# Kernel tuning notes

Measured on AMD Instinct MI355X. Metric: run time of the kernel, lower is better.

Reference implementation:

```python
import jax, jax.numpy as jnp
import numpy as np

B_SZ, L, H, P = 8, 8192, 1024, 64  # batch, seq, d_inner, ssm_size
CONJ_SYM = True
DT_MIN, DT_MAX, DT_FLOOR = 1e-3, 1e-1, 1e-4


def setup_inputs() -> dict:
    key = jax.random.key(0)
    ks = jax.random.split(key, 8)
    u = jax.random.normal(ks[0], (B_SZ, L, H), dtype=jnp.float32)
    h_real = jnp.zeros((B_SZ, P), dtype=jnp.float32)
    h_imag = jnp.zeros((B_SZ, P), dtype=jnp.float32)
    # HiPPO-like stable init: Re(Lambda) = -0.5, Im(Lambda) = pi*k
    A_real = -0.5 * jnp.ones((P,), dtype=jnp.float32)
    A_imag = jnp.pi * jnp.arange(P, dtype=jnp.float32)
    local_P = 2 * P if CONJ_SYM else P
    b_scale = np.sqrt(1.0 / local_P).astype(np.float32)
    c_scale = np.sqrt(1.0 / H).astype(np.float32)
    B_real = jax.random.normal(ks[1], (P, H), dtype=jnp.float32) * b_scale
    B_imag = jax.random.normal(ks[2], (P, H), dtype=jnp.float32) * b_scale
    C_real = jax.random.normal(ks[3], (H, P), dtype=jnp.float32) * c_scale
    C_imag = jax.random.normal(ks[4], (H, P), dtype=jnp.float32) * c_scale
    D = jax.random.normal(ks[5], (H,), dtype=jnp.float32)
    # torch init: dt = exp(U(log dt_min, log dt_max)).clamp(dt_floor); inv_dt = dt + log(-expm1(-dt))
    log_dt = jax.random.uniform(ks[6], (P,), dtype=jnp.float32) \
        * (np.log(DT_MAX) - np.log(DT_MIN)) + np.log(DT_MIN)
    dt0 = jnp.clip(jnp.exp(log_dt), DT_FLOOR, None)
    inv_dt = dt0 + jnp.log(-jnp.expm1(-dt0))
    return {"u": u, "h_real": h_real, "h_imag": h_imag,
            "A_real": A_real, "A_imag": A_imag,
            "B_real": B_real, "B_imag": B_imag,
            "C_real": C_real, "C_imag": C_imag,
            "D": D, "inv_dt": inv_dt}


def reference(u, h_real, h_imag, A_real, A_imag, B_real, B_imag,
              C_real, C_imag, D, inv_dt):
    A = A_real + 1j * A_imag            # (P,)
    Bm = B_real + 1j * B_imag           # (P, H)
    Cm = C_real + 1j * C_imag           # (H, P)
    dt = jax.nn.softplus(inv_dt)        # step_rescale = 1.0
    # bilinear discretization
    den = 1.0 - (dt / 2.0) * A
    dA = (1.0 + (dt / 2.0) * A) / den   # (P,)
    dB = (dt / den)[:, None] * Bm       # (P, H)
    # input projection: Bu[b,l,p] = sum_h dB[p,h] * u[b,l,h]
    Bu = jnp.einsum('blh,ph->blp', u, dB)              # complex64 (B, L, P)
    h0 = h_real + 1j * h_imag                          # (B, P)
    Bu = Bu.at[:, 0].add(dA * h0)                      # fold initial state in
    a = jnp.broadcast_to(dA, Bu.shape)
    def combine(e1, e2):
        a1, b1 = e1
        a2, b2 = e2
        return a2 * a1, a2 * b1 + b2
    _, hs = jax.lax.associative_scan(combine, (a, Bu), axis=1)  # (B, L, P)
    yc = jnp.einsum('blp,hp->blh', hs, Cm)
    scale = 2.0 if CONJ_SYM else 1.0
    y = scale * yc.real + D * u
    h_last = hs[:, -1]
    return y, h_last.real, h_last.imag
```

## Files before the change

### kernel.cpp

```cpp
#include <hip/hip_runtime.h>

typedef unsigned short ushort_t;
typedef short s8v __attribute__((ext_vector_type(8)));
typedef unsigned short ushort8 __attribute__((ext_vector_type(8)));
typedef float floatx4 __attribute__((ext_vector_type(4)));

#define MFMA16(a, b, c) __builtin_amdgcn_mfma_f32_16x16x32_bf16((a), (b), (c), 0, 0, 0)

static constexpr int B_SZ = 8;
static constexpr int L = 8192;
static constexpr int H = 1024;
static constexpr int M_TOT = B_SZ * L;
static constexpr int S_CH = 128;
static constexpr int NC = L / S_CH;

__device__ inline ushort_t f2bf(float f) {
    union { float f; unsigned u; } v; v.f = f;
    unsigned r = v.u + 0x7fffu + ((v.u >> 16) & 1u);
    return (ushort_t)(r >> 16);
}

__device__ inline unsigned cvtpk(float lo, float hi) {
    unsigned r;
    asm("v_cvt_pk_bf16_f32 %0, %1, %2" : "=v"(r) : "v"(lo), "v"(hi));
    return r;
}

typedef union { s8v v; unsigned u[4]; } u32x4;

__device__ inline void gload_lds16(const void* g, void* l) {
    __builtin_amdgcn_global_load_lds(
        (const __attribute__((address_space(1))) void*)g,
        (__attribute__((address_space(3))) void*)l, 16, 0, 0);
}

__global__ void params_kernel(const float* __restrict__ A_real,
                              const float* __restrict__ A_imag,
                              const float* __restrict__ inv_dt,
                              float* __restrict__ params,
                              float* __restrict__ dApow) {
    int p = threadIdx.x;
    float x = inv_dt[p];
    float dt = (x > 20.f) ? x : log1pf(expf(x));
    float ar = A_real[p], ai = A_imag[p];
    float dr = 1.f - 0.5f * dt * ar;
    float di = -0.5f * dt * ai;
    float inv = 1.f / fmaf(dr, dr, di * di);
    float nr = 1.f + 0.5f * dt * ar, ni = 0.5f * dt * ai;
    float dAr = (nr * dr + ni * di) * inv;
    float dAi = (ni * dr - nr * di) * inv;
    params[p]       = dAr;
    params[64 + p]  = dAi;
    params[128 + p] = dt * dr * inv;
    params[192 + p] = -dt * di * inv;
    float pr = 1.f, pi = 0.f;
    dApow[2 * p] = 1.f; dApow[2 * p + 1] = 0.f;
    for (int k = 1; k <= S_CH; k++) {
        float npr = pr * dAr - pi * dAi;
        float npi = pr * dAi + pi * dAr;
        pr = npr; pi = npi;
        dApow[k * 128 + 2 * p]     = pr;
        dApow[k * 128 + 2 * p + 1] = pi;
    }
}

__global__ void build_w(const float* __restrict__ Br, const float* __restrict__ Bi,
                        const float* __restrict__ Cr, const float* __restrict__ Ci,
                        const float* __restrict__ params,
                        ushort_t* __restrict__ W1T, ushort_t* __restrict__ CeffT) {
    int t = blockIdx.x * 256 + threadIdx.x;
    if (t < 128 * 1024) {
        int n = t >> 10, k = t & 1023;
        int p = n >> 1;
        float sr = params[128 + p], si = params[192 + p];
        float br = Br[p * 1024 + k], bi = Bi[p * 1024 + k];
        float v = (n & 1) ? (sr * bi + si * br) : (sr * br - si * bi);
        W1T[t] = f2bf(v);
    } else {
        int t2 = t - 128 * 1024;
        int ct_ti = t2 >> 9, g = t2 & 511;
        int ct = ct_ti >> 2, ti = ct_ti & 3;
        int n = g >> 2;
        int h = ct * 128 + n;
        int qq = (g & 3) ^ ((n >> 1) & 3);
        int kb = ti * 32 + qq * 8;
        ushort8 o;
        #pragma unroll
        for (int e = 0; e < 8; e++) {
            int k = kb + e;
            int p = k >> 1;
            float v = (k & 1) ? -2.f * Ci[h * 64 + p] : 2.f * Cr[h * 64 + p];
            o[e] = f2bf(v);
        }
        *(ushort8*)&CeffT[t2 * 8] = o;
    }
}

__global__ __launch_bounds__(256) void gemm1s(const float* __restrict__ u,
                                              const ushort_t* __restrict__ W1T,
                                              const float* __restrict__ params,
                                              const float* __restrict__ dApow,
                                              float* __restrict__ hloc,
                                              float* __restrict__ endbuf) {
    __shared__ __align__(16) char smem[65536];
    float* bus = (float*)smem;
    int tid = threadIdx.x;
    int wave = tid >> 6, lane = tid & 63;
    int q = lane >> 4, mn = lane & 15;
    size_t row0 = (size_t)blockIdx.x * 128;

    int srA = lane >> 3;
    int sinA = (((lane & 7) ^ srA) << 4);
    int srB = lane >> 2;
    int sinB = (lane & 3) << 4;

    floatx4 acc[2][8] = {};

    int r0 = wave * 32 + mn;
    int maskA = (r0 & 7) << 4;
    int ya0 = r0 * 128 + q * 32;
    int ya1 = (r0 + 16) * 128 + q * 32;

    #define STAGE1(buf, kk)                                                     \
        do {                                                                    \
            _Pragma("unroll")                                                   \
            for (int i_ = 0; i_ < 4; i_++) {                                    \
                int c_ = i_ * 4 + wave;                                         \
                const char* g_ = (const char*)u +                               \
                    (row0 + c_ * 8 + srA) * 4096 + (kk) * 4 + sinA;             \
                gload_lds16(g_, smem + (buf) * 16384 + c_ * 1024);              \
            }                                                                   \
            _Pragma("unroll")                                                   \
            for (int i_ = 0; i_ < 2; i_++) {                                    \
                int c_ = i_ * 4 + wave;                                         \
                const char* g_ = (const char*)W1T +                             \
                    (size_t)(c_ * 16 + srB) * 2048 + (kk) * 2 + sinB;           \
                gload_lds16(g_, smem + 32768 + (buf) * 8192 + c_ * 1024);       \
            }                                                                   \
        } while (0)

    STAGE1(0, 0);
    __syncthreads();
    int cur = 0;
    for (int t = 0; t < 32; t++) {
        if (t < 31) STAGE1(cur ^ 1, (t + 1) * 32);
        const char* abase = smem + cur * 16384;
        floatx4 v00 = *(const floatx4*)(abase + (ya0 ^ maskA));
        floatx4 v01 = *(const floatx4*)(abase + ((ya0 + 16) ^ maskA));
        floatx4 v10 = *(const floatx4*)(abase + (ya1 ^ maskA));
        floatx4 v11 = *(const floatx4*)(abase + ((ya1 + 16) ^ maskA));
        u32x4 a0, a1;
        a0.u[0] = cvtpk(v00[0], v00[1]); a0.u[1] = cvtpk(v00[2], v00[3]);
        a0.u[2] = cvtpk(v01[0], v01[1]); a0.u[3] = cvtpk(v01[2], v01[3]);
        a1.u[0] = cvtpk(v10[0], v10[1]); a1.u[1] = cvtpk(v10[2], v10[3]);
        a1.u[2] = cvtpk(v11[0], v11[1]); a1.u[3] = cvtpk(v11[2], v11[3]);
        const ushort_t* bb = (const ushort_t*)(smem + 32768 + cur * 8192);
        #pragma unroll
        for (int j = 0; j < 8; j++) {
            s8v bf = *(const s8v*)(bb + (j * 16 + mn) * 32 + q * 8);
            acc[0][j] = MFMA16(a0.v, bf, acc[0][j]);
            acc[1][j] = MFMA16(a1.v, bf, acc[1][j]);
        }
        __syncthreads();
        cur ^= 1;
    }
    #undef STAGE1

    #pragma unroll
    for (int i = 0; i < 2; i++)
        #pragma unroll
        for (int j = 0; j < 8; j++)
            #pragma unroll
            for (int reg = 0; reg < 4; reg++) {
                int row = wave * 32 + i * 16 + q * 4 + reg;
                bus[row * 128 + j * 16 + mn] = acc[i][j][reg];
            }
    __syncthreads();

    float dAr = params[lane], dAi = params[64 + lane];
    float hr = 0.f, hi = 0.f;
    int base = wave * 32 * 128 + 2 * lane;
    #pragma unroll 8
    for (int t = 0; t < 32; t++) {
        float2 v = *(float2*)&bus[base + t * 128];
        float nhr = fmaf(dAr, hr, fmaf(-dAi, hi, v.x));
        float nhi = fmaf(dAr, hi, fmaf(dAi, hr, v.y));
        hr = nhr; hi = nhi;
        *(float2*)&bus[base + t * 128] = make_float2(hr, hi);
    }
    __syncthreads();

    float a32r = dApow[32 * 128 + 2 * lane], a32i = dApow[32 * 128 + 2 * lane + 1];
    float cr = 0.f, ci = 0.f;
    for (int w2 = 0; w2 < wave; w2++) {
        float2 e = *(float2*)&bus[(w2 * 32 + 31) * 128 + 2 * lane];
        float tr = fmaf(a32r, cr, fmaf(-a32i, ci, e.x));
        float ti = fmaf(a32r, ci, fmaf(a32i, cr, e.y));
        cr = tr; ci = ti;
    }

    float* gbase = hloc + (row0 + wave * 32) * 128 + 2 * lane;
    float lr = 0.f, li = 0.f;
    float pr = dAr, pi = dAi;
    #pragma unroll 8
    for (int t = 0; t < 32; t++) {
        float2 v = *(float2*)&bus[base + t * 128];
        float orr = v.x + pr * cr - pi * ci;
        float oi  = v.y + pr * ci + pi * cr;
        *(float2*)(gbase + (size_t)t * 128) = make_float2(orr, oi);
        lr = orr; li = oi;
        float npr = pr * dAr - pi * dAi;
        float npi = pr * dAi + pi * dAr;
        pr = npr; pi = npi;
    }
    if (wave == 3) {
        float* e = endbuf + (size_t)blockIdx.x * 128 + 2 * lane;
        e[0] = lr; e[1] = li;
    }
}

__global__ void scan_carry(const float* __restrict__ endbuf,
                           const float* __restrict__ dApow,
                           const float* __restrict__ h0r,
                           const float* __restrict__ h0i,
                           float* __restrict__ carry) {
    int t = blockIdx.x * 64 + threadIdx.x;
    int b = t >> 6, p = t & 63;
    float aSr = dApow[S_CH * 128 + 2 * p], aSi = dApow[S_CH * 128 + 2 * p + 1];
    float cr = h0r[b * 64 + p], ci = h0i[b * 64 + p];
    #pragma unroll
    for (int half = 0; half < 2; half++) {
        float2 e[32];
        #pragma unroll
        for (int c = 0; c < 32; c++)
            e[c] = *(const float2*)(endbuf + ((size_t)b * NC + half * 32 + c) * 128 + 2 * p);
        #pragma unroll
        for (int c = 0; c < 32; c++) {
            int cc = half * 32 + c;
            *(float2*)(carry + ((size_t)b * NC + cc) * 128 + 2 * p) = make_float2(cr, ci);
            float nr = fmaf(aSr, cr, fmaf(-aSi, ci, e[c].x));
            float ni = fmaf(aSr, ci, fmaf(aSi, cr, e[c].y));
            cr = nr; ci = ni;
        }
    }
}

__global__ __launch_bounds__(256, 4) void gemm2t(const float* __restrict__ hloc,
                                                 const ushort_t* __restrict__ CeffT,
                                                 const float* __restrict__ u,
                                                 const float* __restrict__ D,
                                                 const float* __restrict__ dApow,
                                                 const float* __restrict__ carry,
                                                 float* __restrict__ y,
                                                 float* __restrict__ out_hlast) {
    __shared__ __align__(16) char smem[64 * 132 * 4];
    ushort_t* Blds = (ushort_t*)smem;
    float* ldsF = (float*)smem;
    int tid = threadIdx.x;
    int w = tid >> 6, lane = tid & 63;
    int q = lane >> 4, mn = lane & 15;
    int swz = q ^ ((mn >> 1) & 3);
    size_t row0 = (size_t)blockIdx.x * 64;
    int b = (int)(row0 >> 13);
    int l0 = (int)(row0 & (L - 1));
    int c = l0 >> 7;

    int seq = w * 16 + mn;
    int l = l0 + seq;
    int kp = (l & (S_CH - 1)) + 1;
    const float* hrow = hloc + (row0 + seq) * 128;
    const float* prow = dApow + (size_t)kp * 128;
    const float* crow = carry + ((size_t)b * NC + c) * 128;
    bool last = (l == L - 1);

    u32x4 Bf[4];
    #pragma unroll
    for (int kt = 0; kt < 4; kt++) {
        int kb = kt * 32 + q * 8;
        float4 h0 = *(const float4*)(hrow + kb);
        float4 h1 = *(const float4*)(hrow + kb + 4);
        float4 p0 = *(const float4*)(prow + kb);
        float4 p1 = *(const float4*)(prow + kb + 4);
        float4 c0 = *(const float4*)(crow + kb);
        float4 c1 = *(const float4*)(crow + kb + 4);
        float f0 = h0.x + p0.x * c0.x - p0.y * c0.y;
        float f1 = h0.y + p0.x * c0.y + p0.y * c0.x;
        float f2 = h0.z + p0.z * c0.z - p0.w * c0.w;
        float f3 = h0.w + p0.z * c0.w + p0.w * c0.z;
        float f4 = h1.x + p1.x * c1.x - p1.y * c1.y;
        float f5 = h1.y + p1.x * c1.y + p1.y * c1.x;
        float f6 = h1.z + p1.z * c1.z - p1.w * c1.w;
        float f7 = h1.w + p1.z * c1.w + p1.w * c1.z;
        Bf[kt].u[0] = cvtpk(f0, f1); Bf[kt].u[1] = cvtpk(f2, f3);
        Bf[kt].u[2] = cvtpk(f4, f5); Bf[kt].u[3] = cvtpk(f6, f7);
        if (last) {
            int pb = kb >> 1;
            out_hlast[b * 64 + pb]     = f0; out_hlast[512 + b * 64 + pb]     = f1;
            out_hlast[b * 64 + pb + 1] = f2; out_hlast[512 + b * 64 + pb + 1] = f3;
            out_hlast[b * 64 + pb + 2] = f4; out_hlast[512 + b * 64 + pb + 2] = f5;
            out_hlast[b * 64 + pb + 3] = f6; out_hlast[512 + b * 64 + pb + 3] = f7;
        }
    }

    int erow_b = w * 16 + (lane >> 5);
    int es4 = lane & 31;

    for (int ct = 0; ct < 8; ct++) {
        const float* ub = u + ct * 128 + es4 * 4;
        float4 uv0 = *(const float4*)(ub + (row0 + erow_b + 0) * 1024);
        float4 uv1 = *(const float4*)(ub + (row0 + erow_b + 2) * 1024);
        float4 uv2 = *(const float4*)(ub + (row0 + erow_b + 4) * 1024);
        float4 uv3 = *(const float4*)(ub + (row0 + erow_b + 6) * 1024);
        float4 dvv = *(const float4*)(D + ct * 128 + es4 * 4);

        if (ct) __syncthreads();
        {
            const ushort_t* gsrc = CeffT + (size_t)ct * 16384 + w * 512 + lane * 8;
            ushort_t* ldst = Blds + w * 512;
            #pragma unroll
            for (int it = 0; it < 8; it++)
                gload_lds16(gsrc + it * 2048, ldst + it * 2048);
        }
        __syncthreads();
        floatx4 acc[8] = {};
        #pragma unroll
        for (int kt = 0; kt < 4; kt++) {
            int bofs = kt * 4096 + swz * 8;
            #pragma unroll
            for (int j = 0; j < 8; j++) {
                s8v af = *(const s8v*)&Blds[bofs + (j * 16 + mn) * 32];
                acc[j] = MFMA16(af, Bf[kt].v, acc[j]);
            }
        }
        __syncthreads();
        #pragma unroll
        for (int j = 0; j < 8; j++)
            *(floatx4*)&ldsF[(size_t)seq * 132 + j * 16 + q * 4] = acc[j];
        __syncthreads();
        #pragma unroll
        for (int i = 0; i < 8; i++) {
            int row = erow_b + i * 2;
            float4 fv = *(const float4*)&ldsF[(size_t)row * 132 + es4 * 4];
            float4 uvv = (i == 0) ? uv0 : (i == 1) ? uv1 : (i == 2) ? uv2 :
                         (i == 3) ? uv3 :
                         *(const float4*)(ub + (row0 + row) * 1024);
            float4 o;
            o.x = fv.x + dvv.x * uvv.x;
            o.y = fv.y + dvv.y * uvv.y;
            o.z = fv.z + dvv.z * uvv.z;
            o.w = fv.w + dvv.w * uvv.w;
            *(float4*)(y + (row0 + row) * 1024 + ct * 128 + es4 * 4) = o;
        }
    }
}

extern "C" void kernel_launch(void* const* d_in, const int* in_sizes, int n_in,
                              void* d_out, int out_size, void* d_ws, size_t ws_size,
                              hipStream_t stream) {
    const float* u      = (const float*)d_in[0];
    const float* h_r    = (const float*)d_in[1];
    const float* h_i    = (const float*)d_in[2];
    const float* A_real = (const float*)d_in[3];
    const float* A_imag = (const float*)d_in[4];
    const float* B_real = (const float*)d_in[5];
    const float* B_imag = (const float*)d_in[6];
    const float* C_real = (const float*)d_in[7];
    const float* C_imag = (const float*)d_in[8];
    const float* D      = (const float*)d_in[9];
    const float* inv_dt = (const float*)d_in[10];
    float* out = (float*)d_out;

    float* wsf       = (float*)d_ws;
    float* P_params  = wsf;
    float* P_dApow   = wsf + 1024;
    float* P_carry   = wsf + 1024 + 16640;
    float* P_end     = P_carry + 65536;
    ushort_t* P_W1T  = (ushort_t*)(P_end + 65536);
    ushort_t* P_Ceff = P_W1T + 128 * 1024;
    float* P_Bu      = (float*)(P_Ceff + 1024 * 128);

    params_kernel<<<1, 64, 0, stream>>>(A_real, A_imag, inv_dt, P_params, P_dApow);
    build_w<<<576, 256, 0, stream>>>(B_real, B_imag, C_real, C_imag, P_params, P_W1T, P_Ceff);
    gemm1s<<<M_TOT / 128, 256, 0, stream>>>(u, P_W1T, P_params, P_dApow, P_Bu, P_end);
    scan_carry<<<8, 64, 0, stream>>>(P_end, P_dApow, h_r, h_i, P_carry);
    gemm2t<<<M_TOT / 64, 256, 0, stream>>>(P_Bu, P_Ceff, u, D, P_dApow, P_carry,
                                           out, out + (size_t)M_TOT * H);
}
```

Before: 595.1 us.

## Halve scan chunk to 64 rows to double gemm1 blocks and occupancy

Shrinks the chunk size from 128 to 64 sequence positions, so the input-projection GEMM block handles 64 rows, uses half the LDS and accumulators, and launches twice as many blocks with a 4-blocks-per-CU launch bound. The intra-block scan, carry scan (now 128 chunks per batch), gemm2 chunk index and workspace offsets are updated to match. The aim is more parallelism and occupancy for the memory-bound first GEMM. The cost is that the W1 tile is reloaded per 64 rows rather than per 128, and the serial carry scan gets twice as long.

```diff
diff --git a/kernel.cpp b/kernel.cpp
--- a/kernel.cpp
+++ b/kernel.cpp
@@ -11,7 +11,7 @@
 static constexpr int L = 8192;
 static constexpr int H = 1024;
 static constexpr int M_TOT = B_SZ * L;
-static constexpr int S_CH = 128;
+static constexpr int S_CH = 64;
 static constexpr int NC = L / S_CH;
 
 __device__ inline ushort_t f2bf(float f) {
@@ -96,46 +96,45 @@
     }
 }
 
-__global__ __launch_bounds__(256) void gemm1s(const float* __restrict__ u,
-                                              const ushort_t* __restrict__ W1T,
-                                              const float* __restrict__ params,
-                                              const float* __restrict__ dApow,
-                                              float* __restrict__ hloc,
-                                              float* __restrict__ endbuf) {
-    __shared__ __align__(16) char smem[65536];
+__global__ __launch_bounds__(256, 4) void gemm1s(const float* __restrict__ u,
+                                                 const ushort_t* __restrict__ W1T,
+                                                 const float* __restrict__ params,
+                                                 const float* __restrict__ dApow,
+                                                 float* __restrict__ hloc,
+                                                 float* __restrict__ endbuf) {
+    __shared__ __align__(16) char smem[32768];
     float* bus = (float*)smem;
     int tid = threadIdx.x;
     int wave = tid >> 6, lane = tid & 63;
     int q = lane >> 4, mn = lane & 15;
-    size_t row0 = (size_t)blockIdx.x * 128;
+    size_t row0 = (size_t)blockIdx.x * 64;
 
     int srA = lane >> 3;
     int sinA = (((lane & 7) ^ srA) << 4);
     int srB = lane >> 2;
     int sinB = (lane & 3) << 4;
 
-    floatx4 acc[2][8] = {};
-
-    int r0 = wave * 32 + mn;
+    floatx4 acc[8] = {};
+
+    int r0 = wave * 16 + mn;
     int maskA = (r0 & 7) << 4;
     int ya0 = r0 * 128 + q * 32;
-    int ya1 = (r0 + 16) * 128 + q * 32;
 
     #define STAGE1(buf, kk)                                                     \
         do {                                                                    \
             _Pragma("unroll")                                                   \
-            for (int i_ = 0; i_ < 4; i_++) {                                    \
+            for (int i_ = 0; i_ < 2; i_++) {                                    \
                 int c_ = i_ * 4 + wave;                                         \
                 const char* g_ = (const char*)u +                               \
                     (row0 + c_ * 8 + srA) * 4096 + (kk) * 4 + sinA;             \
-                gload_lds16(g_, smem + (buf) * 16384 + c_ * 1024);              \
+                gload_lds16(g_, smem + (buf) * 8192 + c_ * 1024);               \
             }                                                                   \
             _Pragma("unroll")                                                   \
             for (int i_ = 0; i_ < 2; i_++) {                                    \
                 int c_ = i_ * 4 + wave;                                         \
                 const char* g_ = (const char*)W1T +                             \
                     (size_t)(c_ * 16 + srB) * 2048 + (kk) * 2 + sinB;           \
-                gload_lds16(g_, smem + 32768 + (buf) * 8192 + c_ * 1024);       \
+                gload_lds16(g_, smem + 16384 + (buf) * 8192 + c_ * 1024);       \
             }                                                                   \
         } while (0)
 
@@ -144,22 +143,17 @@
     int cur = 0;
     for (int t = 0; t < 32; t++) {
         if (t < 31) STAGE1(cur ^ 1, (t + 1) * 32);
-        const char* abase = smem + cur * 16384;
+        const char* abase = smem + cur * 8192;
         floatx4 v00 = *(const floatx4*)(abase + (ya0 ^ maskA));
         floatx4 v01 = *(const floatx4*)(abase + ((ya0 + 16) ^ maskA));
-        floatx4 v10 = *(const floatx4*)(abase + (ya1 ^ maskA));
-        floatx4 v11 = *(const floatx4*)(abase + ((ya1 + 16) ^ maskA));
-        u32x4 a0, a1;
+        u32x4 a0;
         a0.u[0] = cvtpk(v00[0], v00[1]); a0.u[1] = cvtpk(v00[2], v00[3]);
         a0.u[2] = cvtpk(v01[0], v01[1]); a0.u[3] = cvtpk(v01[2], v01[3]);
-        a1.u[0] = cvtpk(v10[0], v10[1]); a1.u[1] = cvtpk(v10[2], v10[3]);
-        a1.u[2] = cvtpk(v11[0], v11[1]); a1.u[3] = cvtpk(v11[2], v11[3]);
-        const ushort_t* bb = (const ushort_t*)(smem + 32768 + cur * 8192);
+        const ushort_t* bb = (const ushort_t*)(smem + 16384 + cur * 8192);
         #pragma unroll
         for (int j = 0; j < 8; j++) {
             s8v bf = *(const s8v*)(bb + (j * 16 + mn) * 32 + q * 8);
-            acc[0][j] = MFMA16(a0.v, bf, acc[0][j]);
-            acc[1][j] = MFMA16(a1.v, bf, acc[1][j]);
+            acc[j] = MFMA16(a0.v, bf, acc[j]);
         }
         __syncthreads();
         cur ^= 1;
@@ -167,21 +161,19 @@
     #undef STAGE1
 
     #pragma unroll
-    for (int i = 0; i < 2; i++)
-        #pragma unroll
-        for (int j = 0; j < 8; j++)
-            #pragma unroll
-            for (int reg = 0; reg < 4; reg++) {
-                int row = wave * 32 + i * 16 + q * 4 + reg;
-                bus[row * 128 + j * 16 + mn] = acc[i][j][reg];
-            }
+    for (int j = 0; j < 8; j++)
+        #pragma unroll
+        for (int reg = 0; reg < 4; reg++) {
+            int row = wave * 16 + q * 4 + reg;
+            bus[row * 128 + j * 16 + mn] = acc[j][reg];
+        }
     __syncthreads();
 
     float dAr = params[lane], dAi = params[64 + lane];
     float hr = 0.f, hi = 0.f;
-    int base = wave * 32 * 128 + 2 * lane;
+    int base = wave * 16 * 128 + 2 * lane;
     #pragma unroll 8
-    for (int t = 0; t < 32; t++) {
+    for (int t = 0; t < 16; t++) {
         float2 v = *(float2*)&bus[base + t * 128];
         float nhr = fmaf(dAr, hr, fmaf(-dAi, hi, v.x));
         float nhi = fmaf(dAr, hi, fmaf(dAi, hr, v.y));
@@ -190,20 +182,20 @@
     }
     __syncthreads();
 
-    float a32r = dApow[32 * 128 + 2 * lane], a32i = dApow[32 * 128 + 2 * lane + 1];
+    float a16r = dApow[16 * 128 + 2 * lane], a16i = dApow[16 * 128 + 2 * lane + 1];
     float cr = 0.f, ci = 0.f;
     for (int w2 = 0; w2 < wave; w2++) {
-        float2 e = *(float2*)&bus[(w2 * 32 + 31) * 128 + 2 * lane];
-        float tr = fmaf(a32r, cr, fmaf(-a32i, ci, e.x));
-        float ti = fmaf(a32r, ci, fmaf(a32i, cr, e.y));
+        float2 e = *(float2*)&bus[(w2 * 16 + 15) * 128 + 2 * lane];
+        float tr = fmaf(a16r, cr, fmaf(-a16i, ci, e.x));
+        float ti = fmaf(a16r, ci, fmaf(a16i, cr, e.y));
         cr = tr; ci = ti;
     }
 
-    float* gbase = hloc + (row0 + wave * 32) * 128 + 2 * lane;
+    float* gbase = hloc + (row0 + wave * 16) * 128 + 2 * lane;
     float lr = 0.f, li = 0.f;
     float pr = dAr, pi = dAi;
     #pragma unroll 8
-    for (int t = 0; t < 32; t++) {
+    for (int t = 0; t < 16; t++) {
         float2 v = *(float2*)&bus[base + t * 128];
         float orr = v.x + pr * cr - pi * ci;
         float oi  = v.y + pr * ci + pi * cr;
@@ -229,14 +221,14 @@
     float aSr = dApow[S_CH * 128 + 2 * p], aSi = dApow[S_CH * 128 + 2 * p + 1];
     float cr = h0r[b * 64 + p], ci = h0i[b * 64 + p];
     #pragma unroll
-    for (int half = 0; half < 2; half++) {
+    for (int qu = 0; qu < 4; qu++) {
         float2 e[32];
         #pragma unroll
         for (int c = 0; c < 32; c++)
-            e[c] = *(const float2*)(endbuf + ((size_t)b * NC + half * 32 + c) * 128 + 2 * p);
+            e[c] = *(const float2*)(endbuf + ((size_t)b * NC + qu * 32 + c) * 128 + 2 * p);
         #pragma unroll
         for (int c = 0; c < 32; c++) {
-            int cc = half * 32 + c;
+            int cc = qu * 32 + c;
             *(float2*)(carry + ((size_t)b * NC + cc) * 128 + 2 * p) = make_float2(cr, ci);
             float nr = fmaf(aSr, cr, fmaf(-aSi, ci, e[c].x));
             float ni = fmaf(aSr, ci, fmaf(aSi, cr, e[c].y));
@@ -263,7 +255,7 @@
     size_t row0 = (size_t)blockIdx.x * 64;
     int b = (int)(row0 >> 13);
     int l0 = (int)(row0 & (L - 1));
-    int c = l0 >> 7;
+    int c = l0 >> 6;
 
     int seq = w * 16 + mn;
     int l = l0 + seq;
@@ -374,14 +366,14 @@
     float* P_params  = wsf;
     float* P_dApow   = wsf + 1024;
     float* P_carry   = wsf + 1024 + 16640;
-    float* P_end     = P_carry + 65536;
-    ushort_t* P_W1T  = (ushort_t*)(P_end + 65536);
+    float* P_end     = P_carry + 131072;
+    ushort_t* P_W1T  = (ushort_t*)(P_end + 131072);
     ushort_t* P_Ceff = P_W1T + 128 * 1024;
     float* P_Bu      = (float*)(P_Ceff + 1024 * 128);
 
     params_kernel<<<1, 64, 0, stream>>>(A_real, A_imag, inv_dt, P_params, P_dApow);
     build_w<<<576, 256, 0, stream>>>(B_real, B_imag, C_real, C_imag, P_params, P_W1T, P_Ceff);
-    gemm1s<<<M_TOT / 128, 256, 0, stream>>>(u, P_W1T, P_params, P_dApow, P_Bu, P_end);
+    gemm1s<<<M_TOT / 64, 256, 0, stream>>>(u, P_W1T, P_params, P_dApow, P_Bu, P_end);
     scan_carry<<<8, 64, 0, stream>>>(P_end, P_dApow, h_r, h_i, P_carry);
     gemm2t<<<M_TOT / 64, 256, 0, stream>>>(P_Bu, P_Ceff, u, D, P_dApow, P_carry,
                                            out, out + (size_t)M_TOT * H);
```

New measurement: 592.7 us. Within noise of the previous version (-0.4%).
